# Optimization experiments

Hardware: AMD Instinct MI355X
Metric: run time of the kernel (lower is better)

## Reference

```python
import jax, jax.numpy as jnp
import numpy as np

SOS = 1
H = 1024   # hidden_size
V = 32000  # vocab_size
B = 64     # batch
S = 50     # encoder (source) length
T = 25     # decode steps (target length)


def setup_inputs() -> dict:
    key = jax.random.key(0)
    ks = jax.random.split(key, 16)
    s = 1.0 / np.sqrt(H)

    def u(k, shape):
        return jax.random.uniform(k, shape, jnp.float32, -s, s)

    return {
        "encoder_outputs": jax.random.normal(ks[0], (B, S, H), jnp.float32),
        "encoder_hidden": jax.random.normal(ks[1], (1, B, H), jnp.float32),
        "target_tensor": jax.random.randint(ks[2], (B, T), 0, V),
        "emb": jax.random.normal(ks[3], (V, H), jnp.float32),       # nn.Embedding
        "Wa": u(ks[4], (H, H)), "ba": u(ks[5], (H,)),               # attention query proj
        "Ua": u(ks[6], (H, H)), "bu": u(ks[7], (H,)),               # attention key proj
        "Va": u(ks[8], (H, 1)), "bv": u(ks[9], (1,)),               # attention score vector
        "W_ih": u(ks[10], (3 * H, 2 * H)), "b_ih": u(ks[11], (3 * H,)),  # GRU input weights
        "W_hh": u(ks[12], (3 * H, H)), "b_hh": u(ks[13], (3 * H,)),     # GRU hidden weights
        "Wout": u(ks[14], (V, H)), "bout": u(ks[15], (V,)),         # output linear
    }


def reference(encoder_outputs, encoder_hidden, target_tensor, emb,
              Wa, ba, Ua, bu, Va, bv, W_ih, b_ih, W_hh, b_hh, Wout, bout):
    # Bahdanau key projection is independent of the decode step: precompute once.
    keys_proj = encoder_outputs @ Ua.T + bu        # [B, S, H]
    h0 = encoder_hidden[0]                         # [B, H]

    # Teacher forcing: input at step i is SOS then target[:, :-1]. (Dropout in eval mode = identity.)
    sos = jnp.full((B, 1), SOS, dtype=target_tensor.dtype)
    tokens = jnp.concatenate([sos, target_tensor[:, :-1]], axis=1).T  # [T, B]

    def step(h, tok):
        x_emb = emb[tok]                                         # [B, H]
        q = h @ Wa.T + ba                                        # [B, H] (query = hidden)
        scores = jnp.tanh(q[:, None, :] + keys_proj) @ Va        # [B, S, 1]
        w = jax.nn.softmax(scores[..., 0] + bv[0], axis=-1)      # [B, S]
        context = jnp.einsum('bs,bsh->bh', w, encoder_outputs)   # [B, H]
        x = jnp.concatenate([x_emb, context], axis=-1)           # [B, 2H]
        gx = x @ W_ih.T + b_ih                                   # [B, 3H]
        gh = h @ W_hh.T + b_hh                                   # [B, 3H]
        rx, zx, nx = jnp.split(gx, 3, axis=-1)                   # PyTorch gate order r,z,n
        rh, zh, nh = jnp.split(gh, 3, axis=-1)
        r = jax.nn.sigmoid(rx + rh)
        z = jax.nn.sigmoid(zx + zh)
        n = jnp.tanh(nx + r * nh)
        h_new = (1.0 - z) * n + z * h
        logits = h_new @ Wout.T + bout                           # [B, V]
        return h_new, logits

    _, logits = jax.lax.scan(step, h0, tokens)                   # [T, B, V]
    return jnp.transpose(logits, (1, 0, 2))                      # [B, T, V]
```

## Files before the change

### kernel.cpp

```cpp
#include <hip/hip_runtime.h>
#include <hip/hip_bf16.h>

#define BB_ 64
#define SS_ 50
#define TT_ 25
#define HH_ 1024
#define VV_ 32000

typedef __bf16 bf16x8 __attribute__((ext_vector_type(8)));
typedef float f32x4 __attribute__((ext_vector_type(4)));
typedef unsigned long long u64;

__device__ __forceinline__ unsigned short f2b(float f) {
  unsigned u = __float_as_uint(f);
  u = (u + 0x7FFFu + ((u >> 16) & 1u)) >> 16;
  return (unsigned short)u;
}
__device__ __forceinline__ float b2f_(unsigned short s) {
  return __uint_as_float((unsigned)s << 16);
}
__device__ __forceinline__ float fast_tanh(float x) {
  float e = __expf(2.f * x);
  return 1.f - 2.f / (e + 1.f);
}
__device__ __forceinline__ float fast_sigmoid(float x) {
  return 1.f / (1.f + __expf(-x));
}
__device__ __forceinline__ void gload16(const void* g, void* l) {
  __builtin_amdgcn_global_load_lds((const __attribute__((address_space(1))) void*)g,
                                   (__attribute__((address_space(3))) void*)l, 16, 0, 0);
}
__device__ __forceinline__ bf16x8 ldb8(const unsigned short* p) {
  return *(const bf16x8*)p;
}

__device__ __forceinline__ void cstf(float* p, float v) {
  __hip_atomic_store(p, v, __ATOMIC_RELAXED, __HIP_MEMORY_SCOPE_AGENT);
}
__device__ __forceinline__ void cst4(unsigned* p, unsigned v) {
  __hip_atomic_store(p, v, __ATOMIC_RELAXED, __HIP_MEMORY_SCOPE_AGENT);
}
__device__ __forceinline__ unsigned cldu(const unsigned* p) {
  return __hip_atomic_load(p, __ATOMIC_RELAXED, __HIP_MEMORY_SCOPE_AGENT);
}

#define W_HR(c, j)   (cnt + ((c) * 64 + (j)) * 32)
#define W_CTX(c, j)  (cnt + (256 + (c) * 64 + (j)) * 32)
#define W_QR(c, p)   (cnt + (512 + (c) * 16 + (p)) * 32)
#define W_GH(c, p)   (cnt + (576 + (c) * 48 + (p)) * 32)
#define W_MINI(b, k) (cnt + (768 + (b) * 4 + (k)) * 32)
#define CNT_DWORDS 32768

__global__ __launch_bounds__(256) void cvt_bf16(const float* __restrict__ src,
                                                unsigned short* __restrict__ dst, long n) {
  long i = ((long)blockIdx.x * 256 + threadIdx.x) * 4;
  if (i >= n) return;
  float4 v = *(const float4*)(src + i);
  *(ushort4*)(dst + i) = make_ushort4(f2b(v.x), f2b(v.y), f2b(v.z), f2b(v.w));
}

__global__ __launch_bounds__(256) void embed_gather(const int* __restrict__ tgt,
                                                    const float* __restrict__ emb,
                                                    unsigned short* __restrict__ X) {
  long idx = ((long)blockIdx.x * 256 + threadIdx.x) * 4;
  if (idx >= (long)1600 * HH_) return;
  int col = (int)(idx & (HH_ - 1));
  int r = (int)(idx >> 10);
  int t = r % 25;
  int tok = (t == 0) ? 1 : tgt[r - 1];
  float4 v = *(const float4*)(emb + (long)tok * HH_ + col);
  *(ushort4*)(X + idx) = make_ushort4(f2b(v.x), f2b(v.y), f2b(v.z), f2b(v.w));
}

__global__ __launch_bounds__(256) void init_h(const float* __restrict__ eh,
                                              unsigned short* __restrict__ HBROT,
                                              unsigned* __restrict__ cnt) {
  if (blockIdx.x == 0) {
    for (int k = threadIdx.x; k < CNT_DWORDS; k += 256) cnt[k] = 0;
  }
  int i = (blockIdx.x * 256 + threadIdx.x) * 4;
  if (i >= BB_ * HH_) return;
  float4 v = *(const float4*)(eh + i);
  *(ushort4*)(HBROT + i) = make_ushort4(f2b(v.x), f2b(v.y), f2b(v.z), f2b(v.w));
}

__global__ __launch_bounds__(256) void gemm128_bt(
    const unsigned short* __restrict__ A, const unsigned short* __restrict__ W,
    const float* __restrict__ bias, float* __restrict__ out, long ldo,
    int Mtiles, int ldw, int Mvalid) {
  __shared__ __align__(16) unsigned short As[128 * 32];
  __shared__ __align__(16) unsigned short Bs[128 * 32];
  int nwg = gridDim.x;
  int orig = blockIdx.x;
  int xcd = orig & 7, lid = orig >> 3;
  int qq = nwg >> 3, rr = nwg & 7;
  int wgid = (xcd < rr ? xcd * (qq + 1) : rr * (qq + 1) + (xcd - rr) * qq) + lid;
  int m0 = (wgid % Mtiles) * 128;
  int n0 = (wgid / Mtiles) * 128;
  int tid = threadIdx.x;
  int w = tid >> 6, l = tid & 63;
  int srow = tid >> 2, scg = tid & 3;
  int mw = (w & 1) * 64, nw = (w >> 1) * 64;

  const unsigned short* Ag0 = A + (long)(m0 + srow) * 1024 + scg * 8;
  const unsigned short* Ag1 = Ag0 + 64 * 1024;
  const unsigned short* Wg0 = W + (long)(n0 + srow) * ldw + scg * 8;
  const unsigned short* Wg1 = Wg0 + (long)64 * ldw;
  unsigned short* lA0 = As + tid * 8;
  unsigned short* lA1 = As + 2048 + tid * 8;
  unsigned short* lB0 = Bs + tid * 8;
  unsigned short* lB1 = Bs + 2048 + tid * 8;

  f32x4 zero = {0.f, 0.f, 0.f, 0.f};
  f32x4 acc[4][4];
#pragma unroll
  for (int i = 0; i < 4; ++i)
#pragma unroll
    for (int j = 0; j < 4; ++j) acc[i][j] = zero;

  for (int k0 = 0; k0 < 1024; k0 += 32) {
    __syncthreads();
    gload16(Ag0 + k0, lA0);
    gload16(Ag1 + k0, lA1);
    gload16(Wg0 + k0, lB0);
    gload16(Wg1 + k0, lB1);
    __syncthreads();
    bf16x8 af[4], bg[4];
#pragma unroll
    for (int mt = 0; mt < 4; ++mt)
      af[mt] = ldb8(As + (mw + mt * 16 + (l & 15)) * 32 + (l >> 4) * 8);
#pragma unroll
    for (int nt = 0; nt < 4; ++nt)
      bg[nt] = ldb8(Bs + (nw + nt * 16 + (l & 15)) * 32 + (l >> 4) * 8);
#pragma unroll
    for (int mt = 0; mt < 4; ++mt)
#pragma unroll
      for (int nt = 0; nt < 4; ++nt)
        acc[mt][nt] = __builtin_amdgcn_mfma_f32_16x16x32_bf16(af[mt], bg[nt], acc[mt][nt], 0, 0, 0);
  }

  int lr = (l >> 4) * 4, lc = l & 15;
#pragma unroll
  for (int nt = 0; nt < 4; ++nt) {
    int col = n0 + nw + nt * 16 + lc;
    float bv = bias[col];
#pragma unroll
    for (int mt = 0; mt < 4; ++mt) {
#pragma unroll
      for (int r = 0; r < 4; ++r) {
        int m = m0 + mw + mt * 16 + lr + r;
        if (m < Mvalid) out[(long)m * ldo + col] = acc[mt][nt][r] + bv;
      }
    }
  }
}

__global__ __launch_bounds__(256) void decode_loop(
    const unsigned short* __restrict__ WaB, const unsigned short* __restrict__ WhhB,
    const unsigned short* __restrict__ WihB, const float* __restrict__ ba,
    const float* __restrict__ bhh, const float* __restrict__ Va,
    const unsigned short* __restrict__ KEYSB, const unsigned short* __restrict__ ENCB,
    const float* __restrict__ GA, const float* __restrict__ ehid,
    float* __restrict__ QROT, float* __restrict__ GHROT, float* __restrict__ SCROT,
    unsigned short* __restrict__ CTXROT, unsigned short* __restrict__ HBROT,
    unsigned short* __restrict__ HALLB, unsigned* __restrict__ cnt) {
  __shared__ __align__(16) char AsC[16 * 2048];
  __shared__ float qs[1024];
  __shared__ float vas[1024];
  __shared__ float wgt[64];

  const int tid = threadIdx.x, bid = blockIdx.x;
  const int wv = tid >> 6, l = tid & 63;
  const int lc = l & 15, hi = l >> 4, ko = hi * 8, lr4 = hi * 4;
  const int xcd = bid & 7, lxb = bid >> 3;
  const int mt_ = lxb & 3, cg = lxb >> 2;
  const int qcls = xcd >> 1;

  const int hidx = xcd * 8 + cg;
  const int cidx = (xcd & 1) * 32 + lxb;
  const int qidx = (xcd & 1) * 8 + cg;
  const int gidx = (xcd - 2) * 8 + cg;

  const int m1 = mt_ * 16;
  const int nch = xcd * 32 + cg * 4 + wv;
  const int n1 = nch * 16;
  const bool isq = (n1 < 1024);
  const unsigned short* B1 = isq ? WaB + (long)(n1 + lc) * 1024 + ko
                                 : WhhB + (long)(n1 - 1024 + lc) * 1024 + ko;
  float* o1 = isq ? QROT + n1 : GHROT + (n1 - 1024);
  const long ldo1 = isq ? 1024 : 3072;
  const long slot1 = isq ? (long)BB_ * 1024 : (long)BB_ * 3072;
  const float bv1 = isq ? ba[n1 + lc] : bhh[n1 - 1024 + lc];

  const int b2 = xcd * 8 + cg;
  const int jq = mt_ * 4 + wv;
  const int c2 = mt_ * 256 + tid;

  const int m3 = mt_ * 16, n3 = (xcd * 8 + cg) * 16;
  const unsigned short* Bg0 = WihB + (long)(n3 + lc) * 2048 + 1024 + ko;
  const unsigned short* Bg1 = Bg0 + (long)1024 * 2048;
  const unsigned short* Bg2 = Bg0 + (long)2048 * 2048;
  const int ig = n3 + lc;
  float hreg[4];
  if (tid < 64) {
#pragma unroll
    for (int r = 0; r < 4; ++r) hreg[r] = ehid[(long)(m3 + lr4 + r) * HH_ + ig];
  }

#pragma unroll
  for (int j = 0; j < 4; ++j) vas[tid + j * 256] = Va[tid + j * 256];

  const f32x4 zero = {0.f, 0.f, 0.f, 0.f};

  for (int t = 0; t < TT_; ++t) {
    const unsigned ep = (unsigned)(t + 1);
    if (tid < 64) {
      const unsigned* w = W_HR(mt_, tid);
      while (cldu(w) < (unsigned)t) __builtin_amdgcn_s_sleep(1);
    }
    __syncthreads();

    {
      const unsigned short* hbase = HBROT + (long)t * (BB_ * 1024);
#pragma unroll
      for (int i = 0; i < 16; ++i) {
        u64 v = *((const u64*)(hbase + (long)(m1 + i) * 1024) + tid);
        *(u64*)(AsC + ((i * 2048 + tid * 8) ^ ((i & 7) << 4))) = v;
      }
      __syncthreads();
      f32x4 acc = zero;
#pragma unroll 8
      for (int k = 0; k < 1024; k += 32) {
        bf16x8 af = *(const bf16x8*)(AsC + ((lc * 2048 + (k + ko) * 2) ^ ((lc & 7) << 4)));
        acc = __builtin_amdgcn_mfma_f32_16x16x32_bf16(af, ldb8(B1 + k), acc, 0, 0, 0);
      }
#pragma unroll
      for (int r = 0; r < 4; ++r)
        cstf(o1 + (long)t * slot1 + (long)(m1 + lr4 + r) * ldo1 + lc, acc[r] + bv1);
    }
    __syncthreads();
    if (tid == 0) cst4(isq ? W_QR(mt_, qidx) : W_GH(mt_, gidx), ep);
    if (tid < 16) {
      const unsigned* w = W_QR(qcls, tid);
      while (cldu(w) < ep) __builtin_amdgcn_s_sleep(1);
    }
    __syncthreads();

    {
      const float* qsl = QROT + (long)t * (BB_ * 1024) + (long)b2 * 1024;
#pragma unroll
      for (int j = 0; j < 4; ++j)
        qs[tid + j * 256] = qsl[tid + j * 256];
      __syncthreads();
      for (int s = jq; s < SS_; s += 16) {
        const unsigned short* kr = KEYSB + ((long)b2 * SS_ + s) * 1024;
        float p = 0.f;
#pragma unroll
        for (int j = 0; j < 16; ++j) {
          int hh = l + j * 64;
          p += fast_tanh(qs[hh] + b2f_(kr[hh])) * vas[hh];
        }
#pragma unroll
        for (int off = 32; off; off >>= 1) p += __shfl_down(p, off);
        if (l == 0) cstf(SCROT + (long)t * 4096 + b2 * 64 + s, p);
      }
    }
    __syncthreads();
    if (tid == 0) cst4(W_MINI(b2, mt_), ep);
    if (tid < 4) {
      const unsigned* w = W_MINI(b2, tid);
      while (cldu(w) < ep) __builtin_amdgcn_s_sleep(1);
    }
    __syncthreads();

    {
      if (tid < 64) {
        float v = (tid < SS_) ? SCROT[(long)t * 4096 + b2 * 64 + tid] : -1e30f;
        float m = v;
#pragma unroll
        for (int off = 32; off; off >>= 1) m = fmaxf(m, __shfl_down(m, off));
        m = __shfl(m, 0);
        float e = (tid < SS_) ? __expf(v - m) : 0.f;
        float ssum = e;
#pragma unroll
        for (int off = 32; off; off >>= 1) ssum += __shfl_down(ssum, off);
        ssum = __shfl(ssum, 0);
        if (tid < SS_) wgt[tid] = e / ssum;
      }
      __syncthreads();
      {
        const unsigned short* ep_ = ENCB + (long)b2 * SS_ * 1024 + c2;
        float a0 = 0.f;
#pragma unroll 10
        for (int s = 0; s < SS_; ++s)
          a0 += wgt[s] * b2f_(ep_[(long)s * 1024]);
        unsigned hb16 = (unsigned)f2b(a0);
        unsigned ob = (unsigned)__shfl_xor((int)hb16, 1);
        if ((tid & 1) == 0)
          cst4((unsigned*)(CTXROT + (long)t * (BB_ * 1024) + (long)b2 * 1024 + c2), hb16 | (ob << 16));
      }
    }
    __syncthreads();
    if (tid == 0) cst4(W_CTX(qcls, cidx), ep);
    if (tid < 64) {
      const unsigned* w = W_CTX(mt_, tid);
      while (cldu(w) < ep) __builtin_amdgcn_s_sleep(1);
    } else if (tid < 112) {
      const unsigned* w = W_GH(mt_, tid - 64);
      while (cldu(w) < ep) __builtin_amdgcn_s_sleep(1);
    }
    __syncthreads();

    {
      const unsigned short* cbase = CTXROT + (long)t * (BB_ * 1024);
#pragma unroll
      for (int i = 0; i < 16; ++i) {
        u64 v = *((const u64*)(cbase + (long)(m3 + i) * 1024) + tid);
        *(u64*)(AsC + ((i * 2048 + tid * 8) ^ ((i & 7) << 4))) = v;
      }
      __syncthreads();
      if (tid < 64) {
        f32x4 ar = zero, az = zero, an_ = zero;
#pragma unroll 8
        for (int k = 0; k < 1024; k += 32) {
          bf16x8 a = *(const bf16x8*)(AsC + ((lc * 2048 + (k + ko) * 2) ^ ((lc & 7) << 4)));
          ar = __builtin_amdgcn_mfma_f32_16x16x32_bf16(a, ldb8(Bg0 + k), ar, 0, 0, 0);
          az = __builtin_amdgcn_mfma_f32_16x16x32_bf16(a, ldb8(Bg1 + k), az, 0, 0, 0);
          an_ = __builtin_amdgcn_mfma_f32_16x16x32_bf16(a, ldb8(Bg2 + k), an_, 0, 0, 0);
        }
        const float* ghb = GHROT + (long)t * (BB_ * 3072);
        unsigned short* hnb = HBROT + (long)(t + 1) * (BB_ * 1024);
#pragma unroll
        for (int r = 0; r < 4; ++r) {
          int bb = m3 + lr4 + r;
          long rowBT = (long)bb * TT_ + t;
          const float* ga = GA + rowBT * 3072;
          const float* gh = ghb + (long)bb * 3072;
          float rr = fast_sigmoid(ga[ig] + ar[r] + gh[ig]);
          float zz = fast_sigmoid(ga[1024 + ig] + az[r] + gh[1024 + ig]);
          float nn = fast_tanh(ga[2048 + ig] + an_[r] + rr * gh[2048 + ig]);
          float hnew = (1.f - zz) * nn + zz * hreg[r];
          hreg[r] = hnew;
          unsigned hb = (unsigned)f2b(hnew);
          unsigned ob = (unsigned)__shfl_xor((int)hb, 1);
          if ((lc & 1) == 0)
            cst4((unsigned*)(hnb + (long)bb * 1024 + ig), hb | (ob << 16));
          HALLB[rowBT * HH_ + ig] = (unsigned short)hb;
        }
      }
    }
    __syncthreads();
    if (tid == 0) cst4(W_HR(mt_, hidx), ep);
  }
}

extern "C" void kernel_launch(void* const* d_in, const int* in_sizes, int n_in,
                              void* d_out, int out_size, void* d_ws, size_t ws_size,
                              hipStream_t stream) {
  (void)in_sizes; (void)n_in; (void)out_size; (void)ws_size;
  const float* enc  = (const float*)d_in[0];
  const float* ehid = (const float*)d_in[1];
  const int*   tgt  = (const int*)d_in[2];
  const float* emb  = (const float*)d_in[3];
  const float* Wa   = (const float*)d_in[4];
  const float* ba   = (const float*)d_in[5];
  const float* Ua   = (const float*)d_in[6];
  const float* bu   = (const float*)d_in[7];
  const float* Va   = (const float*)d_in[8];
  const float* Wih  = (const float*)d_in[10];
  const float* bih  = (const float*)d_in[11];
  const float* Whh  = (const float*)d_in[12];
  const float* bhh  = (const float*)d_in[13];
  const float* Wout = (const float*)d_in[14];
  const float* bout = (const float*)d_in[15];
  float* out = (float*)d_out;

  char* p = (char*)d_ws;
  auto alloc = [&](size_t bytes) { char* r = p; p += (bytes + 255) & ~(size_t)255; return r; };
  unsigned short* WOUTB = (unsigned short*)alloc((size_t)VV_ * HH_ * 2);
  unsigned short* WIHB  = (unsigned short*)alloc((size_t)3072 * 2048 * 2);
  unsigned short* WHHB  = (unsigned short*)alloc((size_t)3072 * 1024 * 2);
  unsigned short* WAB   = (unsigned short*)alloc((size_t)1024 * 1024 * 2);
  unsigned short* UAB   = (unsigned short*)alloc((size_t)1024 * 1024 * 2);
  unsigned short* ENCB  = (unsigned short*)alloc((size_t)BB_ * SS_ * HH_ * 2);
  unsigned short* XEMB  = (unsigned short*)alloc((size_t)1664 * HH_ * 2);
  unsigned short* HALLB = (unsigned short*)alloc((size_t)1664 * HH_ * 2);
  float* KEYS = (float*)alloc((size_t)BB_ * SS_ * HH_ * 4);
  unsigned short* KEYSB = (unsigned short*)alloc((size_t)BB_ * SS_ * HH_ * 2);
  float* GA   = (float*)alloc((size_t)1600 * 3072 * 4);
  float* QROT  = (float*)alloc((size_t)TT_ * BB_ * 1024 * 4);
  float* GHROT = (float*)alloc((size_t)TT_ * BB_ * 3072 * 4);
  float* SCROT = (float*)alloc((size_t)TT_ * 4096 * 4);
  unsigned short* CTXROT = (unsigned short*)alloc((size_t)TT_ * BB_ * 1024 * 2);
  unsigned short* HBROT  = (unsigned short*)alloc((size_t)(TT_ + 1) * BB_ * 1024 * 2);
  unsigned* CNT = (unsigned*)alloc((size_t)CNT_DWORDS * 4);

  auto cvt = [&](const float* s, unsigned short* d, long n) {
    cvt_bf16<<<dim3((unsigned)((n / 4 + 255) / 256)), dim3(256), 0, stream>>>(s, d, n);
  };
  cvt(Wout, WOUTB, (long)VV_ * HH_);
  cvt(Wih, WIHB, (long)3072 * 2048);
  cvt(Whh, WHHB, (long)3072 * 1024);
  cvt(Wa, WAB, (long)1024 * 1024);
  cvt(Ua, UAB, (long)1024 * 1024);
  cvt(enc, ENCB, (long)BB_ * SS_ * HH_);
  embed_gather<<<dim3(1600 * HH_ / 4 / 256), dim3(256), 0, stream>>>(tgt, emb, XEMB);
  init_h<<<dim3(BB_ * HH_ / 4 / 256), dim3(256), 0, stream>>>(ehid, HBROT, CNT);

  gemm128_bt<<<dim3(25 * 8), dim3(256), 0, stream>>>(ENCB, UAB, bu, KEYS, (long)1024, 25, 1024, 3200);
  cvt(KEYS, KEYSB, (long)BB_ * SS_ * HH_);
  gemm128_bt<<<dim3(13 * 24), dim3(256), 0, stream>>>(XEMB, WIHB, bih, GA, (long)3072, 13, 2048, 1600);

  decode_loop<<<dim3(256), dim3(256), 0, stream>>>(
      WAB, WHHB, WIHB, ba, bhh, Va, KEYSB, ENCB, GA, ehid,
      QROT, GHROT, SCROT, CTXROT, HBROT, HALLB, CNT);

  gemm128_bt<<<dim3(13 * 250), dim3(256), 0, stream>>>(HALLB, WOUTB, bout, out, (long)VV_, 13, 1024, 1600);
}
```

Baseline: 1.666 ms.

## Compute attention per batch row in one block, dropping inter-block score barrier

Attention for each batch row now runs entirely in one block (the mt_==0 block): it computes all 50 scores into shared memory, does the softmax and the full 1024-wide context with vectorized loads. This removes the global SCROT buffer and the W_MINI cross-block barrier. The CTX wait shrinks to 16 producers. The trade-off is that three quarters of the blocks sit idle during attention, so per-block attention work grows fourfold. Spin-wait sleep is also raised from 1 to 2.

```diff
diff --git a/kernel.cpp b/kernel.cpp
--- a/kernel.cpp
+++ b/kernel.cpp
@@ -48,7 +48,6 @@
 #define W_CTX(c, j)  (cnt + (256 + (c) * 64 + (j)) * 32)
 #define W_QR(c, p)   (cnt + (512 + (c) * 16 + (p)) * 32)
 #define W_GH(c, p)   (cnt + (576 + (c) * 48 + (p)) * 32)
-#define W_MINI(b, k) (cnt + (768 + (b) * 4 + (k)) * 32)
 #define CNT_DWORDS 32768
 
 __global__ __launch_bounds__(256) void cvt_bf16(const float* __restrict__ src,
@@ -161,12 +160,13 @@
     const float* __restrict__ bhh, const float* __restrict__ Va,
     const unsigned short* __restrict__ KEYSB, const unsigned short* __restrict__ ENCB,
     const float* __restrict__ GA, const float* __restrict__ ehid,
-    float* __restrict__ QROT, float* __restrict__ GHROT, float* __restrict__ SCROT,
+    float* __restrict__ QROT, float* __restrict__ GHROT,
     unsigned short* __restrict__ CTXROT, unsigned short* __restrict__ HBROT,
     unsigned short* __restrict__ HALLB, unsigned* __restrict__ cnt) {
   __shared__ __align__(16) char AsC[16 * 2048];
   __shared__ float qs[1024];
   __shared__ float vas[1024];
+  __shared__ float scl[64];
   __shared__ float wgt[64];
 
   const int tid = threadIdx.x, bid = blockIdx.x;
@@ -177,9 +177,9 @@
   const int qcls = xcd >> 1;
 
   const int hidx = xcd * 8 + cg;
-  const int cidx = (xcd & 1) * 32 + lxb;
   const int qidx = (xcd & 1) * 8 + cg;
   const int gidx = (xcd - 2) * 8 + cg;
+  const bool isAttn = (mt_ == 0);
 
   const int m1 = mt_ * 16;
   const int nch = xcd * 32 + cg * 4 + wv;
@@ -193,8 +193,6 @@
   const float bv1 = isq ? ba[n1 + lc] : bhh[n1 - 1024 + lc];
 
   const int b2 = xcd * 8 + cg;
-  const int jq = mt_ * 4 + wv;
-  const int c2 = mt_ * 256 + tid;
 
   const int m3 = mt_ * 16, n3 = (xcd * 8 + cg) * 16;
   const unsigned short* Bg0 = WihB + (long)(n3 + lc) * 2048 + 1024 + ko;
@@ -216,7 +214,7 @@
     const unsigned ep = (unsigned)(t + 1);
     if (tid < 64) {
       const unsigned* w = W_HR(mt_, tid);
-      while (cldu(w) < (unsigned)t) __builtin_amdgcn_s_sleep(1);
+      while (cldu(w) < (unsigned)t) __builtin_amdgcn_s_sleep(2);
     }
     __syncthreads();
 
@@ -240,19 +238,20 @@
     }
     __syncthreads();
     if (tid == 0) cst4(isq ? W_QR(mt_, qidx) : W_GH(mt_, gidx), ep);
-    if (tid < 16) {
-      const unsigned* w = W_QR(qcls, tid);
-      while (cldu(w) < ep) __builtin_amdgcn_s_sleep(1);
-    }
-    __syncthreads();
-
-    {
-      const float* qsl = QROT + (long)t * (BB_ * 1024) + (long)b2 * 1024;
-#pragma unroll
-      for (int j = 0; j < 4; ++j)
-        qs[tid + j * 256] = qsl[tid + j * 256];
-      __syncthreads();
-      for (int s = jq; s < SS_; s += 16) {
+
+    if (isAttn) {
+      if (tid < 16) {
+        const unsigned* w = W_QR(qcls, tid);
+        while (cldu(w) < ep) __builtin_amdgcn_s_sleep(2);
+      }
+      __syncthreads();
+      {
+        float4 qv = ((const float4*)(QROT + (long)t * (BB_ * 1024) + (long)b2 * 1024))[tid];
+        qs[tid * 4 + 0] = qv.x; qs[tid * 4 + 1] = qv.y;
+        qs[tid * 4 + 2] = qv.z; qs[tid * 4 + 3] = qv.w;
+      }
+      __syncthreads();
+      for (int s = wv; s < SS_; s += 4) {
         const unsigned short* kr = KEYSB + ((long)b2 * SS_ + s) * 1024;
         float p = 0.f;
 #pragma unroll
@@ -262,20 +261,11 @@
         }
 #pragma unroll
         for (int off = 32; off; off >>= 1) p += __shfl_down(p, off);
-        if (l == 0) cstf(SCROT + (long)t * 4096 + b2 * 64 + s, p);
-      }
-    }
-    __syncthreads();
-    if (tid == 0) cst4(W_MINI(b2, mt_), ep);
-    if (tid < 4) {
-      const unsigned* w = W_MINI(b2, tid);
-      while (cldu(w) < ep) __builtin_amdgcn_s_sleep(1);
-    }
-    __syncthreads();
-
-    {
+        if (l == 0) scl[s] = p;
+      }
+      __syncthreads();
       if (tid < 64) {
-        float v = (tid < SS_) ? SCROT[(long)t * 4096 + b2 * 64 + tid] : -1e30f;
+        float v = (tid < SS_) ? scl[tid] : -1e30f;
         float m = v;
 #pragma unroll
         for (int off = 32; off; off >>= 1) m = fmaxf(m, __shfl_down(m, off));
@@ -289,25 +279,32 @@
       }
       __syncthreads();
       {
-        const unsigned short* ep_ = ENCB + (long)b2 * SS_ * 1024 + c2;
-        float a0 = 0.f;
+        int c0 = tid * 4;
+        const unsigned short* ep_ = ENCB + (long)b2 * SS_ * 1024 + c0;
+        float a0 = 0.f, a1 = 0.f, a2 = 0.f, a3 = 0.f;
 #pragma unroll 10
-        for (int s = 0; s < SS_; ++s)
-          a0 += wgt[s] * b2f_(ep_[(long)s * 1024]);
-        unsigned hb16 = (unsigned)f2b(a0);
-        unsigned ob = (unsigned)__shfl_xor((int)hb16, 1);
-        if ((tid & 1) == 0)
-          cst4((unsigned*)(CTXROT + (long)t * (BB_ * 1024) + (long)b2 * 1024 + c2), hb16 | (ob << 16));
-      }
-    }
-    __syncthreads();
-    if (tid == 0) cst4(W_CTX(qcls, cidx), ep);
-    if (tid < 64) {
+        for (int s = 0; s < SS_; ++s) {
+          ushort4 e4 = *(const ushort4*)(ep_ + (long)s * 1024);
+          float ws_ = wgt[s];
+          a0 += ws_ * b2f_(e4.x); a1 += ws_ * b2f_(e4.y);
+          a2 += ws_ * b2f_(e4.z); a3 += ws_ * b2f_(e4.w);
+        }
+        unsigned u0 = (unsigned)f2b(a0) | ((unsigned)f2b(a1) << 16);
+        unsigned u1 = (unsigned)f2b(a2) | ((unsigned)f2b(a3) << 16);
+        unsigned* cp = (unsigned*)(CTXROT + (long)t * (BB_ * 1024) + (long)b2 * 1024 + c0);
+        cst4(cp, u0);
+        cst4(cp + 1, u1);
+      }
+      __syncthreads();
+      if (tid == 0) cst4(W_CTX(qcls, (xcd & 1) * 8 + cg), ep);
+    }
+
+    if (tid < 16) {
       const unsigned* w = W_CTX(mt_, tid);
-      while (cldu(w) < ep) __builtin_amdgcn_s_sleep(1);
-    } else if (tid < 112) {
+      while (cldu(w) < ep) __builtin_amdgcn_s_sleep(2);
+    } else if (tid >= 64 && tid < 112) {
       const unsigned* w = W_GH(mt_, tid - 64);
-      while (cldu(w) < ep) __builtin_amdgcn_s_sleep(1);
+      while (cldu(w) < ep) __builtin_amdgcn_s_sleep(2);
     }
     __syncthreads();
 
@@ -390,7 +387,6 @@
   float* GA   = (float*)alloc((size_t)1600 * 3072 * 4);
   float* QROT  = (float*)alloc((size_t)TT_ * BB_ * 1024 * 4);
   float* GHROT = (float*)alloc((size_t)TT_ * BB_ * 3072 * 4);
-  float* SCROT = (float*)alloc((size_t)TT_ * 4096 * 4);
   unsigned short* CTXROT = (unsigned short*)alloc((size_t)TT_ * BB_ * 1024 * 2);
   unsigned short* HBROT  = (unsigned short*)alloc((size_t)(TT_ + 1) * BB_ * 1024 * 2);
   unsigned* CNT = (unsigned*)alloc((size_t)CNT_DWORDS * 4);
@@ -413,7 +409,7 @@
 
   decode_loop<<<dim3(256), dim3(256), 0, stream>>>(
       WAB, WHHB, WIHB, ba, bhh, Va, KEYSB, ENCB, GA, ehid,
-      QROT, GHROT, SCROT, CTXROT, HBROT, HALLB, CNT);
+      QROT, GHROT, CTXROT, HBROT, HALLB, CNT);
 
   gemm128_bt<<<dim3(13 * 250), dim3(256), 0, stream>>>(HALLB, WOUTB, bout, out, (long)VV_, 13, 1024, 1600);
 }
```

Measured after the change: 2.947 ms. 76.9% more time.

## Fuse prep kernels, merge pre-GEMMs, and run output GEMM inside decode kernel

Applied to the files above, without the earlier changes.

All bf16 conversions, the embedding gather, the hidden init and the counter clearing are folded into one grid-stride prep kernel. The two pre-loop GEMMs become a single launch, and the key projection now writes bf16 directly, which drops the fp32 KEYS buffer and its conversion pass. The final vocab projection GEMM moves to the tail of the persistent decode kernel: every block waits until all hidden-state flags reach the last step, then processes a contiguous share of the output tiles. This removes several launches and an intermediate round trip. The cost is that the output GEMM runs on only 256 blocks instead of 3250, with a fixed static tile split, and HALLB is now written with paired atomic stores.

```diff
diff --git a/kernel.cpp b/kernel.cpp
--- a/kernel.cpp
+++ b/kernel.cpp
@@ -51,53 +51,14 @@
 #define W_MINI(b, k) (cnt + (768 + (b) * 4 + (k)) * 32)
 #define CNT_DWORDS 32768
 
-__global__ __launch_bounds__(256) void cvt_bf16(const float* __restrict__ src,
-                                                unsigned short* __restrict__ dst, long n) {
-  long i = ((long)blockIdx.x * 256 + threadIdx.x) * 4;
-  if (i >= n) return;
-  float4 v = *(const float4*)(src + i);
-  *(ushort4*)(dst + i) = make_ushort4(f2b(v.x), f2b(v.y), f2b(v.z), f2b(v.w));
-}
-
-__global__ __launch_bounds__(256) void embed_gather(const int* __restrict__ tgt,
-                                                    const float* __restrict__ emb,
-                                                    unsigned short* __restrict__ X) {
-  long idx = ((long)blockIdx.x * 256 + threadIdx.x) * 4;
-  if (idx >= (long)1600 * HH_) return;
-  int col = (int)(idx & (HH_ - 1));
-  int r = (int)(idx >> 10);
-  int t = r % 25;
-  int tok = (t == 0) ? 1 : tgt[r - 1];
-  float4 v = *(const float4*)(emb + (long)tok * HH_ + col);
-  *(ushort4*)(X + idx) = make_ushort4(f2b(v.x), f2b(v.y), f2b(v.z), f2b(v.w));
-}
-
-__global__ __launch_bounds__(256) void init_h(const float* __restrict__ eh,
-                                              unsigned short* __restrict__ HBROT,
-                                              unsigned* __restrict__ cnt) {
-  if (blockIdx.x == 0) {
-    for (int k = threadIdx.x; k < CNT_DWORDS; k += 256) cnt[k] = 0;
-  }
-  int i = (blockIdx.x * 256 + threadIdx.x) * 4;
-  if (i >= BB_ * HH_) return;
-  float4 v = *(const float4*)(eh + i);
-  *(ushort4*)(HBROT + i) = make_ushort4(f2b(v.x), f2b(v.y), f2b(v.z), f2b(v.w));
-}
-
-__global__ __launch_bounds__(256) void gemm128_bt(
+template <bool OBF16>
+__device__ __forceinline__ void gemm_tile(
+    int wgid, int tid, unsigned short* As, unsigned short* Bs,
     const unsigned short* __restrict__ A, const unsigned short* __restrict__ W,
-    const float* __restrict__ bias, float* __restrict__ out, long ldo,
+    const float* __restrict__ bias, void* __restrict__ outp, long ldo,
     int Mtiles, int ldw, int Mvalid) {
-  __shared__ __align__(16) unsigned short As[128 * 32];
-  __shared__ __align__(16) unsigned short Bs[128 * 32];
-  int nwg = gridDim.x;
-  int orig = blockIdx.x;
-  int xcd = orig & 7, lid = orig >> 3;
-  int qq = nwg >> 3, rr = nwg & 7;
-  int wgid = (xcd < rr ? xcd * (qq + 1) : rr * (qq + 1) + (xcd - rr) * qq) + lid;
   int m0 = (wgid % Mtiles) * 128;
   int n0 = (wgid / Mtiles) * 128;
-  int tid = threadIdx.x;
   int w = tid >> 6, l = tid & 63;
   int srow = tid >> 2, scg = tid & 3;
   int mw = (w & 1) * 64, nw = (w >> 1) * 64;
@@ -149,10 +110,79 @@
 #pragma unroll
       for (int r = 0; r < 4; ++r) {
         int m = m0 + mw + mt * 16 + lr + r;
-        if (m < Mvalid) out[(long)m * ldo + col] = acc[mt][nt][r] + bv;
-      }
-    }
-  }
+        if (m < Mvalid) {
+          float v = acc[mt][nt][r] + bv;
+          if (OBF16) ((unsigned short*)outp)[(long)m * ldo + col] = f2b(v);
+          else       ((float*)outp)[(long)m * ldo + col] = v;
+        }
+      }
+    }
+  }
+}
+
+__global__ __launch_bounds__(256) void prep_all(
+    const float* __restrict__ Wout, const float* __restrict__ Wih,
+    const float* __restrict__ Whh, const float* __restrict__ Wa,
+    const float* __restrict__ Ua, const float* __restrict__ enc,
+    const int* __restrict__ tgt, const float* __restrict__ emb,
+    const float* __restrict__ ehid,
+    unsigned short* __restrict__ WOUTB, unsigned short* __restrict__ WIHB,
+    unsigned short* __restrict__ WHHB, unsigned short* __restrict__ WAB,
+    unsigned short* __restrict__ UAB, unsigned short* __restrict__ ENCB,
+    unsigned short* __restrict__ XEMB, unsigned short* __restrict__ HBROT,
+    unsigned* __restrict__ cnt) {
+  const long N0 = 8192000;
+  const long N1 = N0 + 1572864;
+  const long N2 = N1 + 786432;
+  const long N3 = N2 + 262144;
+  const long N4 = N3 + 262144;
+  const long N5 = N4 + 819200;
+  const long N6 = N5 + 409600;
+  const long N7 = N6 + 16384;
+  const long N8 = N7 + 8192;
+  const long stride = (long)gridDim.x * 256;
+  for (long i = (long)blockIdx.x * 256 + threadIdx.x; i < N8; i += stride) {
+    if (i < N5) {
+      const float* s; unsigned short* d; long q;
+      if (i < N0)      { s = Wout; d = WOUTB; q = i; }
+      else if (i < N1) { s = Wih;  d = WIHB;  q = i - N0; }
+      else if (i < N2) { s = Whh;  d = WHHB;  q = i - N1; }
+      else if (i < N3) { s = Wa;   d = WAB;   q = i - N2; }
+      else if (i < N4) { s = Ua;   d = UAB;   q = i - N3; }
+      else             { s = enc;  d = ENCB;  q = i - N4; }
+      float4 v = *(const float4*)(s + q * 4);
+      *(ushort4*)(d + q * 4) = make_ushort4(f2b(v.x), f2b(v.y), f2b(v.z), f2b(v.w));
+    } else if (i < N6) {
+      long idx = (i - N5) * 4;
+      int col = (int)(idx & (HH_ - 1));
+      int r = (int)(idx >> 10);
+      int t = r % 25;
+      int tok = (t == 0) ? 1 : tgt[r - 1];
+      float4 v = *(const float4*)(emb + (long)tok * HH_ + col);
+      *(ushort4*)(XEMB + idx) = make_ushort4(f2b(v.x), f2b(v.y), f2b(v.z), f2b(v.w));
+    } else if (i < N7) {
+      long idx = (i - N6) * 4;
+      float4 v = *(const float4*)(ehid + idx);
+      *(ushort4*)(HBROT + idx) = make_ushort4(f2b(v.x), f2b(v.y), f2b(v.z), f2b(v.w));
+    } else {
+      long q = i - N7;
+      ((uint4*)cnt)[q] = make_uint4(0, 0, 0, 0);
+    }
+  }
+}
+
+__global__ __launch_bounds__(256) void gemm_pre(
+    const unsigned short* __restrict__ ENCB, const unsigned short* __restrict__ UAB,
+    const float* __restrict__ bu, unsigned short* __restrict__ KEYSB,
+    const unsigned short* __restrict__ XEMB, const unsigned short* __restrict__ WIHB,
+    const float* __restrict__ bih, float* __restrict__ GA) {
+  __shared__ __align__(16) unsigned short As[128 * 32];
+  __shared__ __align__(16) unsigned short Bs[128 * 32];
+  int bid = blockIdx.x, tid = threadIdx.x;
+  if (bid < 200)
+    gemm_tile<true>(bid, tid, As, Bs, ENCB, UAB, bu, KEYSB, 1024, 25, 1024, 3200);
+  else
+    gemm_tile<false>(bid - 200, tid, As, Bs, XEMB, WIHB, bih, GA, 3072, 13, 2048, 1600);
 }
 
 __global__ __launch_bounds__(256) void decode_loop(
@@ -163,7 +193,9 @@
     const float* __restrict__ GA, const float* __restrict__ ehid,
     float* __restrict__ QROT, float* __restrict__ GHROT, float* __restrict__ SCROT,
     unsigned short* __restrict__ CTXROT, unsigned short* __restrict__ HBROT,
-    unsigned short* __restrict__ HALLB, unsigned* __restrict__ cnt) {
+    unsigned short* __restrict__ HALLB, unsigned* __restrict__ cnt,
+    const unsigned short* __restrict__ WOUTB, const float* __restrict__ bout,
+    float* __restrict__ out) {
   __shared__ __align__(16) char AsC[16 * 2048];
   __shared__ float qs[1024];
   __shared__ float vas[1024];
@@ -343,15 +375,29 @@
           hreg[r] = hnew;
           unsigned hb = (unsigned)f2b(hnew);
           unsigned ob = (unsigned)__shfl_xor((int)hb, 1);
-          if ((lc & 1) == 0)
-            cst4((unsigned*)(hnb + (long)bb * 1024 + ig), hb | (ob << 16));
-          HALLB[rowBT * HH_ + ig] = (unsigned short)hb;
+          if ((lc & 1) == 0) {
+            unsigned pair = hb | (ob << 16);
+            cst4((unsigned*)(hnb + (long)bb * 1024 + ig), pair);
+            cst4((unsigned*)(HALLB + rowBT * HH_ + ig), pair);
+          }
         }
       }
     }
     __syncthreads();
     if (tid == 0) cst4(W_HR(mt_, hidx), ep);
   }
+
+  {
+    const unsigned* w = W_HR(tid >> 6, tid & 63);
+    while (cldu(w) < (unsigned)TT_) __builtin_amdgcn_s_sleep(1);
+  }
+  __syncthreads();
+  unsigned short* As_t = (unsigned short*)AsC;
+  unsigned short* Bs_t = (unsigned short*)(AsC + 8192);
+  long t0 = ((long)bid * 3250) >> 8;
+  long t1 = ((long)(bid + 1) * 3250) >> 8;
+  for (long tt = t0; tt < t1; ++tt)
+    gemm_tile<false>((int)tt, tid, As_t, Bs_t, HALLB, WOUTB, bout, out, VV_, 13, 1024, 1600);
 }
 
 extern "C" void kernel_launch(void* const* d_in, const int* in_sizes, int n_in,
@@ -385,7 +431,6 @@
   unsigned short* ENCB  = (unsigned short*)alloc((size_t)BB_ * SS_ * HH_ * 2);
   unsigned short* XEMB  = (unsigned short*)alloc((size_t)1664 * HH_ * 2);
   unsigned short* HALLB = (unsigned short*)alloc((size_t)1664 * HH_ * 2);
-  float* KEYS = (float*)alloc((size_t)BB_ * SS_ * HH_ * 4);
   unsigned short* KEYSB = (unsigned short*)alloc((size_t)BB_ * SS_ * HH_ * 2);
   float* GA   = (float*)alloc((size_t)1600 * 3072 * 4);
   float* QROT  = (float*)alloc((size_t)TT_ * BB_ * 1024 * 4);
@@ -395,25 +440,13 @@
   unsigned short* HBROT  = (unsigned short*)alloc((size_t)(TT_ + 1) * BB_ * 1024 * 2);
   unsigned* CNT = (unsigned*)alloc((size_t)CNT_DWORDS * 4);
 
-  auto cvt = [&](const float* s, unsigned short* d, long n) {
-    cvt_bf16<<<dim3((unsigned)((n / 4 + 255) / 256)), dim3(256), 0, stream>>>(s, d, n);
-  };
-  cvt(Wout, WOUTB, (long)VV_ * HH_);
-  cvt(Wih, WIHB, (long)3072 * 2048);
-  cvt(Whh, WHHB, (long)3072 * 1024);
-  cvt(Wa, WAB, (long)1024 * 1024);
-  cvt(Ua, UAB, (long)1024 * 1024);
-  cvt(enc, ENCB, (long)BB_ * SS_ * HH_);
-  embed_gather<<<dim3(1600 * HH_ / 4 / 256), dim3(256), 0, stream>>>(tgt, emb, XEMB);
-  init_h<<<dim3(BB_ * HH_ / 4 / 256), dim3(256), 0, stream>>>(ehid, HBROT, CNT);
-
-  gemm128_bt<<<dim3(25 * 8), dim3(256), 0, stream>>>(ENCB, UAB, bu, KEYS, (long)1024, 25, 1024, 3200);
-  cvt(KEYS, KEYSB, (long)BB_ * SS_ * HH_);
-  gemm128_bt<<<dim3(13 * 24), dim3(256), 0, stream>>>(XEMB, WIHB, bih, GA, (long)3072, 13, 2048, 1600);
+  prep_all<<<dim3(2048), dim3(256), 0, stream>>>(
+      Wout, Wih, Whh, Wa, Ua, enc, tgt, emb, ehid,
+      WOUTB, WIHB, WHHB, WAB, UAB, ENCB, XEMB, HBROT, CNT);
+
+  gemm_pre<<<dim3(512), dim3(256), 0, stream>>>(ENCB, UAB, bu, KEYSB, XEMB, WIHB, bih, GA);
 
   decode_loop<<<dim3(256), dim3(256), 0, stream>>>(
       WAB, WHHB, WIHB, ba, bhh, Va, KEYSB, ENCB, GA, ehid,
-      QROT, GHROT, SCROT, CTXROT, HBROT, HALLB, CNT);
-
-  gemm128_bt<<<dim3(13 * 250), dim3(256), 0, stream>>>(HALLB, WOUTB, bout, out, (long)VV_, 13, 1024, 1600);
-}
+      QROT, GHROT, SCROT, CTXROT, HBROT, HALLB, CNT, WOUTB, bout, out);
+}
```

Result: slower. 1.801 ms (+8.1%).
